# Performance work log

Measured on AMD Instinct MI355X. Metric: run time of the kernel, lower is better.

The kernel has to match this reference:

```python
import jax, jax.numpy as jnp
import numpy as np
from jax import lax

STRIDE = 1
PAD = 1  # module pads 1 on each side whenever padding != 0


def setup_inputs() -> dict:
    key = jax.random.key(0)
    kx, kw, kb = jax.random.split(key, 3)
    x = jax.random.normal(kx, (4096, 4096), dtype=jnp.float32)
    weight = jax.random.normal(kw, (15, 15), dtype=jnp.float32)
    bias = jax.random.normal(kb, (1,), dtype=jnp.float32)
    return {"x": x, "weight": weight, "bias": bias}


def reference(x, weight, bias):
    # Single-channel 2D cross-correlation with constant zero padding of 1 and
    # stride STRIDE, plus a scalar bias. lax.conv_general_dilated computes
    # correlation (no kernel flip), matching the torch corr2d loop exactly.
    out = lax.conv_general_dilated(
        x[None, None, :, :],          # NCHW, N=C=1
        weight[None, None, :, :],      # OIHW, O=I=1
        window_strides=(STRIDE, STRIDE),
        padding=[(PAD, PAD), (PAD, PAD)],
        dimension_numbers=("NCHW", "OIHW", "NCHW"),
    )[0, 0]
    return out + bias[0]
```

## Files before the change

### kernel.cpp

```cpp
#include <hip/hip_runtime.h>

#define IN_N   4096
#define OW     4084
#define KS     15
#define TILE   64
#define XROWS  78
#define XS     88
#define NBX    64
#define NBY    64

typedef __attribute__((ext_vector_type(8))) short     v8s;
typedef __attribute__((ext_vector_type(8))) _Float16  v8h;
typedef __attribute__((ext_vector_type(2))) _Float16  v2h;
typedef __attribute__((ext_vector_type(4))) float     v4f;
typedef __attribute__((ext_vector_type(2))) float     v2f;
typedef __attribute__((ext_vector_type(2))) unsigned  v2u;

__global__ void build_B(const float* __restrict__ w, unsigned short* __restrict__ Bg) {
    int ky = blockIdx.x;
    int e  = threadIdx.x;
    int n = e & 15, quad = e >> 4;
    unsigned short vals[8];
    #pragma unroll
    for (int j = 0; j < 8; ++j) {
        int d = quad * 8 + j - 1 - n;
        _Float16 h = (_Float16)0.0f;
        if (d >= 0 && d < KS) h = (_Float16)w[ky * KS + d];
        union { _Float16 hh; unsigned short u; } cv; cv.hh = h;
        vals[j] = cv.u;
    }
    *(v8s*)(&Bg[(ky * 64 + e) * 8]) = *(const v8s*)vals;
}

__global__ __launch_bounds__(256, 8) void conv2d_mfma3(
    const float* __restrict__ x, const unsigned short* __restrict__ Bg,
    const float* __restrict__ bias, float* __restrict__ out)
{
    __shared__ unsigned short xtile[XROWS * XS] __attribute__((aligned(16)));

    const int tid = threadIdx.x;
    const int bx = blockIdx.x, by = blockIdx.y;
    const int X0 = bx * TILE;
    const int Y0 = by * TILE;
    const bool interior = (bx > 0) & (bx < NBX - 1) & (by > 0) & (by < NBY - 1);

    if (tid < 240) {
        const int tcol = tid % 20;
        const int trow = tid / 20;
        const int c0 = 4 * tcol;
        unsigned short* dst = &xtile[trow * XS + c0];
        if (interior) {
            const float* xr = x + (size_t)(Y0 - 1 + trow) * IN_N + (X0 - 2 + c0);
            #pragma unroll
            for (int i = 0; i < 7; ++i) {
                if (i < 6 || trow < 6) {
                    v2f f01 = *(const v2f*)xr;
                    v2f f23 = *(const v2f*)(xr + 2);
                    v2u p;
                    p.x = __builtin_bit_cast(unsigned, __builtin_amdgcn_cvt_pkrtz(f01.x, f01.y));
                    p.y = __builtin_bit_cast(unsigned, __builtin_amdgcn_cvt_pkrtz(f23.x, f23.y));
                    *(v2u*)dst = p;
                }
                xr  += 12 * (size_t)IN_N;
                dst += 12 * XS;
            }
        } else {
            const int gc0 = X0 - 2 + c0;
            #pragma unroll
            for (int i = 0; i < 7; ++i) {
                int row = trow + 12 * i;
                if (row < XROWS) {
                    int gr = Y0 - 1 + row;
                    float f0 = 0.f, f1 = 0.f, f2 = 0.f, f3 = 0.f;
                    if ((unsigned)gr < (unsigned)IN_N) {
                        const float* xr = x + (size_t)gr * IN_N;
                        if ((unsigned)(gc0 + 0) < (unsigned)IN_N) f0 = xr[gc0 + 0];
                        if ((unsigned)(gc0 + 1) < (unsigned)IN_N) f1 = xr[gc0 + 1];
                        if ((unsigned)(gc0 + 2) < (unsigned)IN_N) f2 = xr[gc0 + 2];
                        if ((unsigned)(gc0 + 3) < (unsigned)IN_N) f3 = xr[gc0 + 3];
                    }
                    v2u p;
                    p.x = __builtin_bit_cast(unsigned, __builtin_amdgcn_cvt_pkrtz(f0, f1));
                    p.y = __builtin_bit_cast(unsigned, __builtin_amdgcn_cvt_pkrtz(f2, f3));
                    *(v2u*)(&xtile[row * XS + c0]) = p;
                }
            }
        }
    }
    __syncthreads();

    const int lane = tid & 63;
    const int wv   = tid >> 6;
    const int m    = lane & 15;
    const int quad = lane >> 4;

    v4f acc[4];
    #pragma unroll
    for (int t = 0; t < 4; ++t) acc[t] = (v4f){0.f, 0.f, 0.f, 0.f};

    const v8h* Bgv = (const v8h*)Bg;
    v8h bcur = Bgv[lane];
    const unsigned short* arow = &xtile[(wv * 16 + m) * XS + quad * 8];

    #pragma unroll
    for (int ky = 0; ky < KS; ++ky) {
        v8h bnext = (ky < KS - 1) ? Bgv[(ky + 1) * 64 + lane] : bcur;
        v8h a0 = *(const v8h*)(arow + 0);
        v8h a1 = *(const v8h*)(arow + 16);
        v8h a2 = *(const v8h*)(arow + 32);
        v8h a3 = *(const v8h*)(arow + 48);
        acc[0] = __builtin_amdgcn_mfma_f32_16x16x32_f16(a0, bcur, acc[0], 0, 0, 0);
        acc[1] = __builtin_amdgcn_mfma_f32_16x16x32_f16(a1, bcur, acc[1], 0, 0, 0);
        acc[2] = __builtin_amdgcn_mfma_f32_16x16x32_f16(a2, bcur, acc[2], 0, 0, 0);
        acc[3] = __builtin_amdgcn_mfma_f32_16x16x32_f16(a3, bcur, acc[3], 0, 0, 0);
        arow += XS;
        bcur = bnext;
    }

    const float bv = bias[0];
    const int orow0 = Y0 + wv * 16 + quad * 4;
    const int ocol0 = X0 + m;
    if (interior | ((bx < NBX - 1) & (by < NBY - 1))) {
        float* o0 = &out[(size_t)orow0 * OW + ocol0];
        #pragma unroll
        for (int t = 0; t < 4; ++t) {
            #pragma unroll
            for (int r = 0; r < 4; ++r)
                o0[(size_t)r * OW + t * 16] = acc[t][r] + bv;
        }
    } else {
        #pragma unroll
        for (int t = 0; t < 4; ++t) {
            int oc = ocol0 + t * 16;
            if (oc < OW) {
                #pragma unroll
                for (int r = 0; r < 4; ++r) {
                    int orow = orow0 + r;
                    if (orow < OW)
                        out[(size_t)orow * OW + oc] = acc[t][r] + bv;
                }
            }
        }
    }
}

extern "C" void kernel_launch(void* const* d_in, const int* in_sizes, int n_in,
                              void* d_out, int out_size, void* d_ws, size_t ws_size,
                              hipStream_t stream) {
    const float* x    = (const float*)d_in[0];
    const float* w    = (const float*)d_in[1];
    const float* bias = (const float*)d_in[2];
    float* out        = (float*)d_out;
    unsigned short* Bg = (unsigned short*)d_ws;

    build_B<<<dim3(KS), dim3(64), 0, stream>>>(w, Bg);
    dim3 grid(NBX, NBY);
    conv2d_mfma3<<<grid, dim3(256), 0, stream>>>(x, Bg, bias, out);
}
```

Before: 141.0 us.

## Give each wave a private halo slice and drop block barrier

```diff
diff --git a/kernel.cpp b/kernel.cpp
--- a/kernel.cpp
+++ b/kernel.cpp
@@ -3,18 +3,16 @@
 #define IN_N   4096
 #define OW     4084
 #define KS     15
-#define TILE   64
-#define XROWS  78
 #define XS     88
+#define WROWS  30
 #define NBX    64
-#define NBY    64
+#define NBY    128
 
 typedef __attribute__((ext_vector_type(8))) short     v8s;
 typedef __attribute__((ext_vector_type(8))) _Float16  v8h;
-typedef __attribute__((ext_vector_type(2))) _Float16  v2h;
 typedef __attribute__((ext_vector_type(4))) float     v4f;
 typedef __attribute__((ext_vector_type(2))) float     v2f;
-typedef __attribute__((ext_vector_type(2))) unsigned  v2u;
+typedef __attribute__((ext_vector_type(4))) unsigned  v4u;
 
 __global__ void build_B(const float* __restrict__ w, unsigned short* __restrict__ Bg) {
     int ky = blockIdx.x;
@@ -32,65 +30,77 @@
     *(v8s*)(&Bg[(ky * 64 + e) * 8]) = *(const v8s*)vals;
 }
 
-__global__ __launch_bounds__(256, 8) void conv2d_mfma3(
+__device__ __forceinline__ unsigned pk(float a, float b) {
+    return __builtin_bit_cast(unsigned, __builtin_amdgcn_cvt_pkrtz(a, b));
+}
+
+__global__ __launch_bounds__(128, 7) void conv2d_mfma4(
     const float* __restrict__ x, const unsigned short* __restrict__ Bg,
     const float* __restrict__ bias, float* __restrict__ out)
 {
-    __shared__ unsigned short xtile[XROWS * XS] __attribute__((aligned(16)));
+    __shared__ unsigned short xtile[2 * WROWS * XS] __attribute__((aligned(16)));
 
-    const int tid = threadIdx.x;
-    const int bx = blockIdx.x, by = blockIdx.y;
-    const int X0 = bx * TILE;
-    const int Y0 = by * TILE;
-    const bool interior = (bx > 0) & (bx < NBX - 1) & (by > 0) & (by < NBY - 1);
+    const int tid  = threadIdx.x;
+    const int lane = tid & 63;
+    const int wv   = tid >> 6;
+    const int bx   = blockIdx.x;
+    const int RT   = blockIdx.y * 2 + wv;
+    const int X0   = bx * 64;
+    const int R0   = RT * 16;
 
-    if (tid < 240) {
-        const int tcol = tid % 20;
-        const int trow = tid / 20;
-        const int c0 = 4 * tcol;
-        unsigned short* dst = &xtile[trow * XS + c0];
+    unsigned short* slice = &xtile[wv * (WROWS * XS)];
+
+    const bool interior = (bx >= 1) & (bx <= 62) & (RT >= 1) & (RT <= 254);
+
+    if (lane < 60) {
+        const int r0 = lane / 10;
+        const int cu = lane % 10;
+        unsigned short* dst = slice + r0 * XS + cu * 8;
         if (interior) {
-            const float* xr = x + (size_t)(Y0 - 1 + trow) * IN_N + (X0 - 2 + c0);
+            const float* xr = x + (size_t)(R0 - 1 + r0) * IN_N + (X0 - 2 + cu * 8);
             #pragma unroll
-            for (int i = 0; i < 7; ++i) {
-                if (i < 6 || trow < 6) {
-                    v2f f01 = *(const v2f*)xr;
-                    v2f f23 = *(const v2f*)(xr + 2);
-                    v2u p;
-                    p.x = __builtin_bit_cast(unsigned, __builtin_amdgcn_cvt_pkrtz(f01.x, f01.y));
-                    p.y = __builtin_bit_cast(unsigned, __builtin_amdgcn_cvt_pkrtz(f23.x, f23.y));
-                    *(v2u*)dst = p;
-                }
-                xr  += 12 * (size_t)IN_N;
-                dst += 12 * XS;
+            for (int i = 0; i < 5; ++i) {
+                v2f f0 = *(const v2f*)(xr + 0);
+                v2f f1 = *(const v2f*)(xr + 2);
+                v2f f2 = *(const v2f*)(xr + 4);
+                v2f f3 = *(const v2f*)(xr + 6);
+                v4u p;
+                p.x = pk(f0.x, f0.y);
+                p.y = pk(f1.x, f1.y);
+                p.z = pk(f2.x, f2.y);
+                p.w = pk(f3.x, f3.y);
+                *(v4u*)dst = p;
+                xr  += 6 * (size_t)IN_N;
+                dst += 6 * XS;
             }
         } else {
-            const int gc0 = X0 - 2 + c0;
+            const int gc0 = X0 - 2 + cu * 8;
             #pragma unroll
-            for (int i = 0; i < 7; ++i) {
-                int row = trow + 12 * i;
-                if (row < XROWS) {
-                    int gr = Y0 - 1 + row;
-                    float f0 = 0.f, f1 = 0.f, f2 = 0.f, f3 = 0.f;
-                    if ((unsigned)gr < (unsigned)IN_N) {
-                        const float* xr = x + (size_t)gr * IN_N;
-                        if ((unsigned)(gc0 + 0) < (unsigned)IN_N) f0 = xr[gc0 + 0];
-                        if ((unsigned)(gc0 + 1) < (unsigned)IN_N) f1 = xr[gc0 + 1];
-                        if ((unsigned)(gc0 + 2) < (unsigned)IN_N) f2 = xr[gc0 + 2];
-                        if ((unsigned)(gc0 + 3) < (unsigned)IN_N) f3 = xr[gc0 + 3];
-                    }
-                    v2u p;
-                    p.x = __builtin_bit_cast(unsigned, __builtin_amdgcn_cvt_pkrtz(f0, f1));
-                    p.y = __builtin_bit_cast(unsigned, __builtin_amdgcn_cvt_pkrtz(f2, f3));
-                    *(v2u*)(&xtile[row * XS + c0]) = p;
+            for (int i = 0; i < 5; ++i) {
+                const int r  = r0 + 6 * i;
+                const int gr = R0 - 1 + r;
+                float f[8];
+                #pragma unroll
+                for (int j = 0; j < 8; ++j) f[j] = 0.0f;
+                if ((unsigned)gr < (unsigned)IN_N) {
+                    const float* xr = x + (size_t)gr * IN_N;
+                    #pragma unroll
+                    for (int j = 0; j < 8; ++j)
+                        if ((unsigned)(gc0 + j) < (unsigned)IN_N) f[j] = xr[gc0 + j];
                 }
+                v4u p;
+                p.x = pk(f[0], f[1]);
+                p.y = pk(f[2], f[3]);
+                p.z = pk(f[4], f[5]);
+                p.w = pk(f[6], f[7]);
+                *(v4u*)(slice + r * XS + cu * 8) = p;
             }
         }
     }
-    __syncthreads();
 
-    const int lane = tid & 63;
-    const int wv   = tid >> 6;
+    asm volatile("s_waitcnt lgkmcnt(0)" ::: "memory");
+    __builtin_amdgcn_sched_barrier(0);
+
     const int m    = lane & 15;
     const int quad = lane >> 4;
 
@@ -99,28 +109,37 @@
     for (int t = 0; t < 4; ++t) acc[t] = (v4f){0.f, 0.f, 0.f, 0.f};
 
     const v8h* Bgv = (const v8h*)Bg;
+    const unsigned short* arow = slice + m * XS + quad * 8;
+
     v8h bcur = Bgv[lane];
-    const unsigned short* arow = &xtile[(wv * 16 + m) * XS + quad * 8];
+    v8h a0 = *(const v8h*)(arow + 0);
+    v8h a1 = *(const v8h*)(arow + 16);
+    v8h a2 = *(const v8h*)(arow + 32);
+    v8h a3 = *(const v8h*)(arow + 48);
 
     #pragma unroll
     for (int ky = 0; ky < KS; ++ky) {
-        v8h bnext = (ky < KS - 1) ? Bgv[(ky + 1) * 64 + lane] : bcur;
-        v8h a0 = *(const v8h*)(arow + 0);
-        v8h a1 = *(const v8h*)(arow + 16);
-        v8h a2 = *(const v8h*)(arow + 32);
-        v8h a3 = *(const v8h*)(arow + 48);
+        const unsigned short* nrow = arow + XS;
+        v8h bn = bcur, n0 = a0, n1 = a1, n2 = a2, n3 = a3;
+        if (ky < KS - 1) {
+            bn = Bgv[(ky + 1) * 64 + lane];
+            n0 = *(const v8h*)(nrow + 0);
+            n1 = *(const v8h*)(nrow + 16);
+            n2 = *(const v8h*)(nrow + 32);
+            n3 = *(const v8h*)(nrow + 48);
+        }
         acc[0] = __builtin_amdgcn_mfma_f32_16x16x32_f16(a0, bcur, acc[0], 0, 0, 0);
         acc[1] = __builtin_amdgcn_mfma_f32_16x16x32_f16(a1, bcur, acc[1], 0, 0, 0);
         acc[2] = __builtin_amdgcn_mfma_f32_16x16x32_f16(a2, bcur, acc[2], 0, 0, 0);
         acc[3] = __builtin_amdgcn_mfma_f32_16x16x32_f16(a3, bcur, acc[3], 0, 0, 0);
-        arow += XS;
-        bcur = bnext;
+        a0 = n0; a1 = n1; a2 = n2; a3 = n3; bcur = bn;
+        arow = nrow;
     }
 
     const float bv = bias[0];
-    const int orow0 = Y0 + wv * 16 + quad * 4;
+    const int orow0 = R0 + quad * 4;
     const int ocol0 = X0 + m;
-    if (interior | ((bx < NBX - 1) & (by < NBY - 1))) {
+    if ((bx < NBX - 1) & (RT < 255)) {
         float* o0 = &out[(size_t)orow0 * OW + ocol0];
         #pragma unroll
         for (int t = 0; t < 4; ++t) {
@@ -155,5 +174,5 @@
 
     build_B<<<dim3(KS), dim3(64), 0, stream>>>(w, Bg);
     dim3 grid(NBX, NBY);
-    conv2d_mfma3<<<grid, dim3(256), 0, stream>>>(x, Bg, bias, out);
+    conv2d_mfma4<<<grid, dim3(128), 0, stream>>>(x, Bg, bias, out);
 }
```

Measured after the change: 156.7 us. 11.1% more time.
